# Kernel optimization log

Hardware: AMD Instinct MI355X
Metric: run time of the kernel (lower is better)

Reference implementation:

```python
import jax, jax.numpy as jnp
import numpy as np

N_NODES = 50000
N_EDGES = 800000
D_FEAT = 128
UNITS = 128


def setup_inputs() -> dict:
    key = jax.random.key(0)
    k1, k2, k3, k4 = jax.random.split(key, 4)
    x = jax.random.normal(k1, (N_NODES, D_FEAT), dtype=jnp.float32)
    source = jax.random.randint(k2, (N_EDGES,), 0, N_NODES, dtype=jnp.int32)
    target = jax.random.randint(k3, (N_EDGES,), 0, N_NODES, dtype=jnp.int32)
    W = jax.random.normal(k4, (D_FEAT, UNITS), dtype=jnp.float32) * (1.0 / np.sqrt(D_FEAT))
    b = jnp.zeros((UNITS,), dtype=jnp.float32)
    return {"x": x, "source": source, "target": target, "W": W, "b": b}


def _degree(idx, n_nodes):
    # in/out degree = segment-sum of unit edge weights; clamp to >= 1 (no self loops)
    deg = jnp.zeros((n_nodes,), dtype=jnp.float32).at[idx].add(1.0)
    return jnp.maximum(deg, 1.0)


def reference(x, source, target, W, b):
    n = x.shape[0]
    # degree_normalization == "in_out": sender scale from out-degree, receiver from in-degree
    sender_scale = jax.lax.rsqrt(_degree(source, n))[:, None]      # [N, 1]
    receiver_scale = jax.lax.rsqrt(_degree(target, n))[:, None]    # [N, 1]
    normalized = sender_scale * x                                  # [N, D]
    source_bcast = normalized[source]                              # [E, D] gather
    pooled = jax.ops.segment_sum(source_bcast, target, num_segments=n)  # [N, D] scatter-add
    pooled = receiver_scale * pooled
    # Dense(units, activation='relu', use_bias=True)
    return jax.nn.relu(pooled @ W + b)
```

## Files before the change

kernel.cpp:

```cpp
#include <hip/hip_runtime.h>
#include <hip/hip_bf16.h>

#define N_FEAT 128
#define EPT 8
#define CHUNK 2048
#define BSHIFT 8
#define MAXRANGE 256
#define CAP 8192
#define LSTR 66

typedef short bf16x8 __attribute__((ext_vector_type(8)));
typedef float f32x4  __attribute__((ext_vector_type(4)));

__device__ __forceinline__ unsigned short f2bf_rtne(float f) {
    unsigned u = __float_as_uint(f);
    u += 0x7fffu + ((u >> 16) & 1u);
    return (unsigned short)(u >> 16);
}
__device__ __forceinline__ float bf2f(unsigned short h) {
    return __uint_as_float((unsigned)h << 16);
}

__global__ __launch_bounds__(256) void scatter_kernel(const int* __restrict__ source,
                                                      const int* __restrict__ target,
                                                      int* __restrict__ curT,
                                                      int* __restrict__ curS,
                                                      unsigned int* __restrict__ pairsT,
                                                      unsigned char* __restrict__ srcB,
                                                      int E, int NB) {
    __shared__ unsigned int   lds_pairs[CHUNK];
    __shared__ unsigned short lds_sp[CHUNK];
    __shared__ int ct[MAXRANGE], cs[MAXRANGE];
    __shared__ int st[MAXRANGE], ss[MAXRANGE];
    __shared__ int gt[MAXRANGE], gs[MAXRANGE];
    int tid = threadIdx.x, b = blockIdx.x;
    int base = b * CHUNK;
    int cnt = E - base; if (cnt > CHUNK) cnt = CHUNK;

    int rs[EPT], rt[EPT];
    ct[tid] = 0; cs[tid] = 0;
    __syncthreads();
    #pragma unroll
    for (int j = 0; j < EPT; ++j) {
        int e = base + j * 256 + tid;
        if (e < E) {
            int s = source[e], t = target[e];
            rs[j] = s; rt[j] = t;
            atomicAdd(&ct[t >> BSHIFT], 1);
            atomicAdd(&cs[s >> BSHIFT], 1);
        }
    }
    __syncthreads();
    int vt = ct[tid], vs = cs[tid];
    st[tid] = vt; ss[tid] = vs;
    __syncthreads();
    #pragma unroll
    for (int off = 1; off < 256; off <<= 1) {
        int t1 = (tid >= off) ? st[tid - off] : 0;
        int t2 = (tid >= off) ? ss[tid - off] : 0;
        __syncthreads();
        st[tid] += t1; ss[tid] += t2;
        __syncthreads();
    }
    int et = st[tid] - vt, es = ss[tid] - vs;
    int gT = 0, gS = 0;
    if (tid < NB) {
        if (vt) gT = atomicAdd(&curT[tid], vt);
        if (vs) gS = atomicAdd(&curS[tid], vs);
    }
    __syncthreads();
    st[tid] = et; ss[tid] = es;
    ct[tid] = et; cs[tid] = es;
    gt[tid] = gT; gs[tid] = gS;
    __syncthreads();
    #pragma unroll
    for (int j = 0; j < EPT; ++j) {
        int e = base + j * 256 + tid;
        if (e < E) {
            int s = rs[j], t = rt[j];
            int k = t >> BSHIFT;
            int p = atomicAdd(&ct[k], 1);
            lds_pairs[p] = (unsigned)s | ((unsigned)t << 16);
            int k2 = s >> BSHIFT;
            int p2 = atomicAdd(&cs[k2], 1);
            lds_sp[p2] = (unsigned short)s;
        }
    }
    __syncthreads();
    for (int i = tid; i < cnt; i += 256) {
        unsigned w = lds_pairs[i];
        int k = w >> 24;
        pairsT[(size_t)k * CAP + gt[k] + (i - st[k])] = w;
        unsigned short sp = lds_sp[i];
        int k2 = sp >> 8;
        srcB[(size_t)k2 * CAP + gs[k2] + (i - ss[k2])] = (unsigned char)sp;
    }
}

__global__ __launch_bounds__(256) void prep_kernel(const unsigned char* __restrict__ srcB,
                                                   const unsigned int* __restrict__ pairsT,
                                                   const int* __restrict__ curT,
                                                   const int* __restrict__ curS,
                                                   const float* __restrict__ x,
                                                   const float* __restrict__ W,
                                                   unsigned short* __restrict__ xb,
                                                   int2* __restrict__ offs,
                                                   int* __restrict__ elist,
                                                   float* __restrict__ ri,
                                                   unsigned short* __restrict__ Whi,
                                                   unsigned short* __restrict__ Wlo,
                                                   int N, int NB) {
    __shared__ int hist[MAXRANGE];
    __shared__ int sb[MAXRANGE];
    __shared__ int excl[MAXRANGE];
    __shared__ int cur[MAXRANGE];
    __shared__ float so_l[MAXRANGE];
    int tid = threadIdx.x, b = blockIdx.x;

    if (b < NB) {
        hist[tid] = 0;
        __syncthreads();
        int cnt = curS[b];
        size_t base = (size_t)b * CAP;
        for (int i = tid; i < cnt; i += 256)
            atomicAdd(&hist[srcB[base + i]], 1);
        __syncthreads();
        {
            int d = hist[tid]; if (d < 1) d = 1;
            so_l[tid] = rsqrtf((float)d);
        }
        __syncthreads();
        int row0 = b << BSHIFT;
        int nrows = N - row0; if (nrows > 256) nrows = 256;
        if (nrows <= 0) return;
        int nf4 = nrows * (N_FEAT / 4);
        const float4* xr = (const float4*)(x + (size_t)row0 * N_FEAT);
        ushort4* xo = (ushort4*)(xb + (size_t)row0 * N_FEAT);
        for (int i = tid; i < nf4; i += 256) {
            float s = so_l[i >> 5];
            float4 v = xr[i];
            xo[i] = make_ushort4(f2bf_rtne(s * v.x), f2bf_rtne(s * v.y),
                                 f2bf_rtne(s * v.z), f2bf_rtne(s * v.w));
        }
    } else if (b < 2 * NB) {
        int bb = b - NB;
        hist[tid] = 0; cur[tid] = 0;
        __syncthreads();
        int cnt = curT[bb];
        int gbase = bb * CAP;
        for (int i = tid; i < cnt; i += 256)
            atomicAdd(&hist[(pairsT[(size_t)gbase + i] >> 16) & 255], 1);
        __syncthreads();
        int deg = hist[tid];
        sb[tid] = deg;
        __syncthreads();
        #pragma unroll
        for (int off = 1; off < 256; off <<= 1) {
            int t = (tid >= off) ? sb[tid - off] : 0;
            __syncthreads();
            sb[tid] += t;
            __syncthreads();
        }
        excl[tid] = sb[tid] - deg;
        __syncthreads();
        int node = (bb << BSHIFT) + tid;
        if (node < N) {
            int st0 = gbase + excl[tid];
            offs[node] = make_int2(st0, st0 + deg);
            int d = deg; if (d < 1) d = 1;
            ri[node] = rsqrtf((float)d);
        }
        for (int i = tid; i < cnt; i += 256) {
            unsigned w = pairsT[(size_t)gbase + i];
            int tl = (w >> 16) & 255;
            int pos = atomicAdd(&cur[tl], 1);
            elist[gbase + excl[tl] + pos] = (int)(w & 0xFFFFu);
        }
    } else {
        int idx = (b - 2 * NB) * 256 + tid;
        int lane = idx & 63;
        int ks = (idx >> 6) & 3;
        int ct2 = idx >> 8;
        int n  = ct2 * 16 + (lane & 15);
        int k0 = ks * 32 + (lane >> 4) * 8;
        unsigned short h[8], l[8];
        #pragma unroll
        for (int j = 0; j < 8; ++j) {
            float w = W[(k0 + j) * N_FEAT + n];
            unsigned short hh = f2bf_rtne(w);
            h[j] = hh;
            l[j] = f2bf_rtne(w - bf2f(hh));
        }
        size_t off = (size_t)idx * 8;
        *(ushort4*)(Whi + off)     = make_ushort4(h[0], h[1], h[2], h[3]);
        *(ushort4*)(Whi + off + 4) = make_ushort4(h[4], h[5], h[6], h[7]);
        *(ushort4*)(Wlo + off)     = make_ushort4(l[0], l[1], l[2], l[3]);
        *(ushort4*)(Wlo + off + 4) = make_ushort4(l[4], l[5], l[6], l[7]);
    }
}

#define ACC_ROW(u, a) { a.x += __uint_as_float((u) << 16); \
                        a.y += __uint_as_float((u) & 0xffff0000u); }

__global__ __launch_bounds__(256) void agg_gemm_kernel(const unsigned short* __restrict__ xb,
                                                       const int* __restrict__ elist,
                                                       const int2* __restrict__ offs,
                                                       const float* __restrict__ ri,
                                                       const unsigned short* __restrict__ Whi,
                                                       const unsigned short* __restrict__ Wlo,
                                                       const float* __restrict__ bias,
                                                       float* __restrict__ out,
                                                       int N) {
    __shared__ unsigned int hi_l[16 * LSTR];
    __shared__ unsigned int lo_l[16 * LSTR];
    int wave = threadIdx.x >> 6;
    int lane = threadIdx.x & 63;
    int quad = lane >> 4;
    int rowbase = blockIdx.x * 16;
    int col = lane * 2;

    #pragma unroll
    for (int i = 0; i < 4; ++i) {
        int r = wave * 4 + i;
        int node = rowbase + r;
        float vx = 0.f, vy = 0.f;
        if (node < N) {
            int2 oe = offs[node];
            int start = __builtin_amdgcn_readfirstlane(oe.x);
            int end   = __builtin_amdgcn_readfirstlane(oe.y);
            float rr = ri[node];
            float2 a0 = make_float2(0.f, 0.f), a1 = a0, a2 = a0, a3 = a0;
            int j = start;
            for (; j + 16 <= end; j += 16) {
                int e0 = elist[j],      e1 = elist[j + 1];
                int e2 = elist[j + 2],  e3 = elist[j + 3];
                int e4 = elist[j + 4],  e5 = elist[j + 5];
                int e6 = elist[j + 6],  e7 = elist[j + 7];
                int e8 = elist[j + 8],  e9 = elist[j + 9];
                int ea = elist[j + 10], eb = elist[j + 11];
                int ec = elist[j + 12], ed = elist[j + 13];
                int ee = elist[j + 14], ef = elist[j + 15];
                unsigned u0 = *(const unsigned*)(xb + (size_t)e0 * N_FEAT + col);
                unsigned u1 = *(const unsigned*)(xb + (size_t)e1 * N_FEAT + col);
                unsigned u2 = *(const unsigned*)(xb + (size_t)e2 * N_FEAT + col);
                unsigned u3 = *(const unsigned*)(xb + (size_t)e3 * N_FEAT + col);
                unsigned u4 = *(const unsigned*)(xb + (size_t)e4 * N_FEAT + col);
                unsigned u5 = *(const unsigned*)(xb + (size_t)e5 * N_FEAT + col);
                unsigned u6 = *(const unsigned*)(xb + (size_t)e6 * N_FEAT + col);
                unsigned u7 = *(const unsigned*)(xb + (size_t)e7 * N_FEAT + col);
                unsigned u8 = *(const unsigned*)(xb + (size_t)e8 * N_FEAT + col);
                unsigned u9 = *(const unsigned*)(xb + (size_t)e9 * N_FEAT + col);
                unsigned ua = *(const unsigned*)(xb + (size_t)ea * N_FEAT + col);
                unsigned ub = *(const unsigned*)(xb + (size_t)eb * N_FEAT + col);
                unsigned uc = *(const unsigned*)(xb + (size_t)ec * N_FEAT + col);
                unsigned ud = *(const unsigned*)(xb + (size_t)ed * N_FEAT + col);
                unsigned ue = *(const unsigned*)(xb + (size_t)ee * N_FEAT + col);
                unsigned uf = *(const unsigned*)(xb + (size_t)ef * N_FEAT + col);
                ACC_ROW(u0, a0) ACC_ROW(u1, a1) ACC_ROW(u2, a2) ACC_ROW(u3, a3)
                ACC_ROW(u4, a0) ACC_ROW(u5, a1) ACC_ROW(u6, a2) ACC_ROW(u7, a3)
                ACC_ROW(u8, a0) ACC_ROW(u9, a1) ACC_ROW(ua, a2) ACC_ROW(ub, a3)
                ACC_ROW(uc, a0) ACC_ROW(ud, a1) ACC_ROW(ue, a2) ACC_ROW(uf, a3)
            }
            for (; j + 8 <= end; j += 8) {
                int e0 = elist[j],     e1 = elist[j + 1];
                int e2 = elist[j + 2], e3 = elist[j + 3];
                int e4 = elist[j + 4], e5 = elist[j + 5];
                int e6 = elist[j + 6], e7 = elist[j + 7];
                unsigned u0 = *(const unsigned*)(xb + (size_t)e0 * N_FEAT + col);
                unsigned u1 = *(const unsigned*)(xb + (size_t)e1 * N_FEAT + col);
                unsigned u2 = *(const unsigned*)(xb + (size_t)e2 * N_FEAT + col);
                unsigned u3 = *(const unsigned*)(xb + (size_t)e3 * N_FEAT + col);
                unsigned u4 = *(const unsigned*)(xb + (size_t)e4 * N_FEAT + col);
                unsigned u5 = *(const unsigned*)(xb + (size_t)e5 * N_FEAT + col);
                unsigned u6 = *(const unsigned*)(xb + (size_t)e6 * N_FEAT + col);
                unsigned u7 = *(const unsigned*)(xb + (size_t)e7 * N_FEAT + col);
                ACC_ROW(u0, a0) ACC_ROW(u1, a1) ACC_ROW(u2, a2) ACC_ROW(u3, a3)
                ACC_ROW(u4, a0) ACC_ROW(u5, a1) ACC_ROW(u6, a2) ACC_ROW(u7, a3)
            }
            for (; j < end; ++j) {
                int e = elist[j];
                unsigned u = *(const unsigned*)(xb + (size_t)e * N_FEAT + col);
                ACC_ROW(u, a0)
            }
            vx = ((a0.x + a1.x) + (a2.x + a3.x)) * rr;
            vy = ((a0.y + a1.y) + (a2.y + a3.y)) * rr;
        }
        unsigned short hx = f2bf_rtne(vx), hy = f2bf_rtne(vy);
        unsigned short lx = f2bf_rtne(vx - bf2f(hx)), ly = f2bf_rtne(vy - bf2f(hy));
        hi_l[r * LSTR + lane] = (unsigned)hx | ((unsigned)hy << 16);
        lo_l[r * LSTR + lane] = (unsigned)lx | ((unsigned)ly << 16);
    }
    __syncthreads();

    bf16x8 Ahi[4], Alo[4];
    int m = lane & 15;
    #pragma unroll
    for (int ks = 0; ks < 4; ++ks) {
        int a = m * LSTR + ks * 16 + quad * 4;
        Ahi[ks] = *(const bf16x8*)(hi_l + a);
        Alo[ks] = *(const bf16x8*)(lo_l + a);
    }
    const bf16x8* BH = (const bf16x8*)Whi;
    const bf16x8* BL = (const bf16x8*)Wlo;

    #pragma unroll
    for (int c = 0; c < 2; ++c) {
        int ct = wave * 2 + c;
        f32x4 acc = {0.f, 0.f, 0.f, 0.f};
        #pragma unroll
        for (int ks = 0; ks < 4; ++ks) {
            bf16x8 bh = BH[(ct * 4 + ks) * 64 + lane];
            bf16x8 bl = BL[(ct * 4 + ks) * 64 + lane];
            acc = __builtin_amdgcn_mfma_f32_16x16x32_bf16(Ahi[ks], bh, acc, 0, 0, 0);
            acc = __builtin_amdgcn_mfma_f32_16x16x32_bf16(Alo[ks], bh, acc, 0, 0, 0);
            acc = __builtin_amdgcn_mfma_f32_16x16x32_bf16(Ahi[ks], bl, acc, 0, 0, 0);
        }
        int colc = ct * 16 + m;
        float bv = bias[colc];
        #pragma unroll
        for (int reg = 0; reg < 4; ++reg) {
            int r = rowbase + quad * 4 + reg;
            if (r < N)
                out[(size_t)r * N_FEAT + colc] = fmaxf(acc[reg] + bv, 0.f);
        }
    }
}

extern "C" void kernel_launch(void* const* d_in, const int* in_sizes, int n_in,
                              void* d_out, int out_size, void* d_ws, size_t ws_size,
                              hipStream_t stream) {
    const float* x      = (const float*)d_in[0];
    const int*   source = (const int*)d_in[1];
    const int*   target = (const int*)d_in[2];
    const float* W      = (const float*)d_in[3];
    const float* bias   = (const float*)d_in[4];
    float*       out    = (float*)d_out;

    const int N = in_sizes[0] / N_FEAT;
    const int E = in_sizes[1];

    const int NB   = (N + MAXRANGE - 1) >> BSHIFT;
    const int NBLK = (E + CHUNK - 1) / CHUNK;

    uintptr_t p = (uintptr_t)d_ws;
    auto carve = [&](size_t bytes) {
        p = (p + 255) & ~(uintptr_t)255;
        uintptr_t r = p;
        p += bytes;
        return (void*)r;
    };
    int*            curs    = (int*)carve((size_t)2 * NB * sizeof(int));
    int*            curT    = curs;
    int*            curS    = curs + NB;
    unsigned int*   pairsT  = (unsigned int*)carve((size_t)NB * CAP * sizeof(unsigned int));
    int*            elist   = (int*)carve((size_t)NB * CAP * sizeof(int));
    unsigned char*  srcB    = (unsigned char*)carve((size_t)NB * CAP);
    float*          ri      = (float*)carve((size_t)N * sizeof(float));
    int2*           offs    = (int2*)carve((size_t)N * sizeof(int2));
    unsigned short* xb      = (unsigned short*)carve((size_t)N * N_FEAT * sizeof(unsigned short));
    unsigned short* Whi     = (unsigned short*)carve((size_t)N_FEAT * N_FEAT * sizeof(unsigned short));
    unsigned short* Wlo     = (unsigned short*)carve((size_t)N_FEAT * N_FEAT * sizeof(unsigned short));
    (void)ws_size; (void)n_in; (void)out_size;

    (void)hipMemsetAsync(curs, 0, (size_t)2 * NB * sizeof(int), stream);

    scatter_kernel<<<NBLK, 256, 0, stream>>>(source, target, curT, curS, pairsT, srcB, E, NB);
    prep_kernel<<<2 * NB + 8, 256, 0, stream>>>(srcB, pairsT, curT, curS, x, W,
                                                xb, offs, elist, ri, Whi, Wlo, N, NB);
    agg_gemm_kernel<<<(N + 15) / 16, 256, 0, stream>>>(xb, elist, offs, ri,
                                                       Whi, Wlo, bias, out, N);
}
```

Before: 153.1 us.

## Count out-degree with global atomics and gather 16-byte rows per lane

The scatter kernel no longer bins source indices into byte buckets. It increments a per-node global out-degree array with atomics, which removes the srcB buffer and the histogram pass in prep. The x prescale/bf16 conversion becomes a separate grid-stride branch reading the degree directly. The aggregation loop now has each quarter-wave handle a different edge, loading 16-byte chunks of a row and combining partial sums with cross-lane shuffles. The trade is contended global atomics and extra shuffle work in exchange for wider gathers and fewer passes.

```diff
diff --git a/kernel.cpp b/kernel.cpp
--- a/kernel.cpp
+++ b/kernel.cpp
@@ -8,6 +8,7 @@
 #define MAXRANGE 256
 #define CAP 8192
 #define LSTR 66
+#define PA_BLOCKS 1024
 
 typedef short bf16x8 __attribute__((ext_vector_type(8)));
 typedef float f32x4  __attribute__((ext_vector_type(4)));
@@ -24,21 +25,19 @@
 __global__ __launch_bounds__(256) void scatter_kernel(const int* __restrict__ source,
                                                       const int* __restrict__ target,
                                                       int* __restrict__ curT,
-                                                      int* __restrict__ curS,
+                                                      int* __restrict__ degS,
                                                       unsigned int* __restrict__ pairsT,
-                                                      unsigned char* __restrict__ srcB,
                                                       int E, int NB) {
-    __shared__ unsigned int   lds_pairs[CHUNK];
-    __shared__ unsigned short lds_sp[CHUNK];
-    __shared__ int ct[MAXRANGE], cs[MAXRANGE];
-    __shared__ int st[MAXRANGE], ss[MAXRANGE];
-    __shared__ int gt[MAXRANGE], gs[MAXRANGE];
+    __shared__ unsigned int lds_pairs[CHUNK];
+    __shared__ int ct[MAXRANGE];
+    __shared__ int st[MAXRANGE];
+    __shared__ int gt[MAXRANGE];
     int tid = threadIdx.x, b = blockIdx.x;
     int base = b * CHUNK;
     int cnt = E - base; if (cnt > CHUNK) cnt = CHUNK;
 
     int rs[EPT], rt[EPT];
-    ct[tid] = 0; cs[tid] = 0;
+    ct[tid] = 0;
     __syncthreads();
     #pragma unroll
     for (int j = 0; j < EPT; ++j) {
@@ -47,43 +46,34 @@
             int s = source[e], t = target[e];
             rs[j] = s; rt[j] = t;
             atomicAdd(&ct[t >> BSHIFT], 1);
-            atomicAdd(&cs[s >> BSHIFT], 1);
-        }
-    }
-    __syncthreads();
-    int vt = ct[tid], vs = cs[tid];
-    st[tid] = vt; ss[tid] = vs;
+            atomicAdd(&degS[s], 1);
+        }
+    }
+    __syncthreads();
+    int vt = ct[tid];
+    st[tid] = vt;
     __syncthreads();
     #pragma unroll
     for (int off = 1; off < 256; off <<= 1) {
         int t1 = (tid >= off) ? st[tid - off] : 0;
-        int t2 = (tid >= off) ? ss[tid - off] : 0;
-        __syncthreads();
-        st[tid] += t1; ss[tid] += t2;
-        __syncthreads();
-    }
-    int et = st[tid] - vt, es = ss[tid] - vs;
-    int gT = 0, gS = 0;
-    if (tid < NB) {
-        if (vt) gT = atomicAdd(&curT[tid], vt);
-        if (vs) gS = atomicAdd(&curS[tid], vs);
-    }
-    __syncthreads();
-    st[tid] = et; ss[tid] = es;
-    ct[tid] = et; cs[tid] = es;
-    gt[tid] = gT; gs[tid] = gS;
+        __syncthreads();
+        st[tid] += t1;
+        __syncthreads();
+    }
+    int et = st[tid] - vt;
+    int gT = 0;
+    if (tid < NB && vt) gT = atomicAdd(&curT[tid], vt);
+    __syncthreads();
+    st[tid] = et; ct[tid] = et; gt[tid] = gT;
     __syncthreads();
     #pragma unroll
     for (int j = 0; j < EPT; ++j) {
         int e = base + j * 256 + tid;
         if (e < E) {
-            int s = rs[j], t = rt[j];
+            int t = rt[j];
             int k = t >> BSHIFT;
             int p = atomicAdd(&ct[k], 1);
-            lds_pairs[p] = (unsigned)s | ((unsigned)t << 16);
-            int k2 = s >> BSHIFT;
-            int p2 = atomicAdd(&cs[k2], 1);
-            lds_sp[p2] = (unsigned short)s;
+            lds_pairs[p] = (unsigned)rs[j] | ((unsigned)t << 16);
         }
     }
     __syncthreads();
@@ -91,16 +81,12 @@
         unsigned w = lds_pairs[i];
         int k = w >> 24;
         pairsT[(size_t)k * CAP + gt[k] + (i - st[k])] = w;
-        unsigned short sp = lds_sp[i];
-        int k2 = sp >> 8;
-        srcB[(size_t)k2 * CAP + gs[k2] + (i - ss[k2])] = (unsigned char)sp;
-    }
-}
-
-__global__ __launch_bounds__(256) void prep_kernel(const unsigned char* __restrict__ srcB,
-                                                   const unsigned int* __restrict__ pairsT,
+    }
+}
+
+__global__ __launch_bounds__(256) void prep_kernel(const unsigned int* __restrict__ pairsT,
                                                    const int* __restrict__ curT,
-                                                   const int* __restrict__ curS,
+                                                   const int* __restrict__ degS,
                                                    const float* __restrict__ x,
                                                    const float* __restrict__ W,
                                                    unsigned short* __restrict__ xb,
@@ -114,36 +100,10 @@
     __shared__ int sb[MAXRANGE];
     __shared__ int excl[MAXRANGE];
     __shared__ int cur[MAXRANGE];
-    __shared__ float so_l[MAXRANGE];
     int tid = threadIdx.x, b = blockIdx.x;
 
     if (b < NB) {
-        hist[tid] = 0;
-        __syncthreads();
-        int cnt = curS[b];
-        size_t base = (size_t)b * CAP;
-        for (int i = tid; i < cnt; i += 256)
-            atomicAdd(&hist[srcB[base + i]], 1);
-        __syncthreads();
-        {
-            int d = hist[tid]; if (d < 1) d = 1;
-            so_l[tid] = rsqrtf((float)d);
-        }
-        __syncthreads();
-        int row0 = b << BSHIFT;
-        int nrows = N - row0; if (nrows > 256) nrows = 256;
-        if (nrows <= 0) return;
-        int nf4 = nrows * (N_FEAT / 4);
-        const float4* xr = (const float4*)(x + (size_t)row0 * N_FEAT);
-        ushort4* xo = (ushort4*)(xb + (size_t)row0 * N_FEAT);
-        for (int i = tid; i < nf4; i += 256) {
-            float s = so_l[i >> 5];
-            float4 v = xr[i];
-            xo[i] = make_ushort4(f2bf_rtne(s * v.x), f2bf_rtne(s * v.y),
-                                 f2bf_rtne(s * v.z), f2bf_rtne(s * v.w));
-        }
-    } else if (b < 2 * NB) {
-        int bb = b - NB;
+        int bb = b;
         hist[tid] = 0; cur[tid] = 0;
         __syncthreads();
         int cnt = curT[bb];
@@ -176,8 +136,8 @@
             int pos = atomicAdd(&cur[tl], 1);
             elist[gbase + excl[tl] + pos] = (int)(w & 0xFFFFu);
         }
-    } else {
-        int idx = (b - 2 * NB) * 256 + tid;
+    } else if (b < NB + 8) {
+        int idx = (b - NB) * 256 + tid;
         int lane = idx & 63;
         int ks = (idx >> 6) & 3;
         int ct2 = idx >> 8;
@@ -196,6 +156,19 @@
         *(ushort4*)(Whi + off + 4) = make_ushort4(h[4], h[5], h[6], h[7]);
         *(ushort4*)(Wlo + off)     = make_ushort4(l[0], l[1], l[2], l[3]);
         *(ushort4*)(Wlo + off + 4) = make_ushort4(l[4], l[5], l[6], l[7]);
+    } else {
+        int pb = b - NB - 8;
+        int total = N * (N_FEAT / 4);
+        const float4* xr = (const float4*)x;
+        ushort4* xo = (ushort4*)xb;
+        for (int i = pb * 256 + tid; i < total; i += PA_BLOCKS * 256) {
+            int row = i >> 5;
+            int d = degS[row]; if (d < 1) d = 1;
+            float s = rsqrtf((float)d);
+            float4 v = xr[i];
+            xo[i] = make_ushort4(f2bf_rtne(s * v.x), f2bf_rtne(s * v.y),
+                                 f2bf_rtne(s * v.z), f2bf_rtne(s * v.w));
+        }
     }
 }
 
@@ -216,14 +189,14 @@
     int wave = threadIdx.x >> 6;
     int lane = threadIdx.x & 63;
     int quad = lane >> 4;
+    int k16  = lane & 15;
     int rowbase = blockIdx.x * 16;
-    int col = lane * 2;
+    const uint4* xr = (const uint4*)xb;
 
     #pragma unroll
     for (int i = 0; i < 4; ++i) {
         int r = wave * 4 + i;
         int node = rowbase + r;
-        float vx = 0.f, vy = 0.f;
         if (node < N) {
             int2 oe = offs[node];
             int start = __builtin_amdgcn_readfirstlane(oe.x);
@@ -232,68 +205,67 @@
             float2 a0 = make_float2(0.f, 0.f), a1 = a0, a2 = a0, a3 = a0;
             int j = start;
             for (; j + 16 <= end; j += 16) {
-                int e0 = elist[j],      e1 = elist[j + 1];
-                int e2 = elist[j + 2],  e3 = elist[j + 3];
-                int e4 = elist[j + 4],  e5 = elist[j + 5];
-                int e6 = elist[j + 6],  e7 = elist[j + 7];
-                int e8 = elist[j + 8],  e9 = elist[j + 9];
-                int ea = elist[j + 10], eb = elist[j + 11];
-                int ec = elist[j + 12], ed = elist[j + 13];
-                int ee = elist[j + 14], ef = elist[j + 15];
-                unsigned u0 = *(const unsigned*)(xb + (size_t)e0 * N_FEAT + col);
-                unsigned u1 = *(const unsigned*)(xb + (size_t)e1 * N_FEAT + col);
-                unsigned u2 = *(const unsigned*)(xb + (size_t)e2 * N_FEAT + col);
-                unsigned u3 = *(const unsigned*)(xb + (size_t)e3 * N_FEAT + col);
-                unsigned u4 = *(const unsigned*)(xb + (size_t)e4 * N_FEAT + col);
-                unsigned u5 = *(const unsigned*)(xb + (size_t)e5 * N_FEAT + col);
-                unsigned u6 = *(const unsigned*)(xb + (size_t)e6 * N_FEAT + col);
-                unsigned u7 = *(const unsigned*)(xb + (size_t)e7 * N_FEAT + col);
-                unsigned u8 = *(const unsigned*)(xb + (size_t)e8 * N_FEAT + col);
-                unsigned u9 = *(const unsigned*)(xb + (size_t)e9 * N_FEAT + col);
-                unsigned ua = *(const unsigned*)(xb + (size_t)ea * N_FEAT + col);
-                unsigned ub = *(const unsigned*)(xb + (size_t)eb * N_FEAT + col);
-                unsigned uc = *(const unsigned*)(xb + (size_t)ec * N_FEAT + col);
-                unsigned ud = *(const unsigned*)(xb + (size_t)ed * N_FEAT + col);
-                unsigned ue = *(const unsigned*)(xb + (size_t)ee * N_FEAT + col);
-                unsigned uf = *(const unsigned*)(xb + (size_t)ef * N_FEAT + col);
-                ACC_ROW(u0, a0) ACC_ROW(u1, a1) ACC_ROW(u2, a2) ACC_ROW(u3, a3)
-                ACC_ROW(u4, a0) ACC_ROW(u5, a1) ACC_ROW(u6, a2) ACC_ROW(u7, a3)
-                ACC_ROW(u8, a0) ACC_ROW(u9, a1) ACC_ROW(ua, a2) ACC_ROW(ub, a3)
-                ACC_ROW(uc, a0) ACC_ROW(ud, a1) ACC_ROW(ue, a2) ACC_ROW(uf, a3)
-            }
-            for (; j + 8 <= end; j += 8) {
-                int e0 = elist[j],     e1 = elist[j + 1];
-                int e2 = elist[j + 2], e3 = elist[j + 3];
-                int e4 = elist[j + 4], e5 = elist[j + 5];
-                int e6 = elist[j + 6], e7 = elist[j + 7];
-                unsigned u0 = *(const unsigned*)(xb + (size_t)e0 * N_FEAT + col);
-                unsigned u1 = *(const unsigned*)(xb + (size_t)e1 * N_FEAT + col);
-                unsigned u2 = *(const unsigned*)(xb + (size_t)e2 * N_FEAT + col);
-                unsigned u3 = *(const unsigned*)(xb + (size_t)e3 * N_FEAT + col);
-                unsigned u4 = *(const unsigned*)(xb + (size_t)e4 * N_FEAT + col);
-                unsigned u5 = *(const unsigned*)(xb + (size_t)e5 * N_FEAT + col);
-                unsigned u6 = *(const unsigned*)(xb + (size_t)e6 * N_FEAT + col);
-                unsigned u7 = *(const unsigned*)(xb + (size_t)e7 * N_FEAT + col);
-                ACC_ROW(u0, a0) ACC_ROW(u1, a1) ACC_ROW(u2, a2) ACC_ROW(u3, a3)
-                ACC_ROW(u4, a0) ACC_ROW(u5, a1) ACC_ROW(u6, a2) ACC_ROW(u7, a3)
-            }
-            for (; j < end; ++j) {
-                int e = elist[j];
-                unsigned u = *(const unsigned*)(xb + (size_t)e * N_FEAT + col);
-                ACC_ROW(u, a0)
-            }
-            vx = ((a0.x + a1.x) + (a2.x + a3.x)) * rr;
-            vy = ((a0.y + a1.y) + (a2.y + a3.y)) * rr;
-        }
-        unsigned short hx = f2bf_rtne(vx), hy = f2bf_rtne(vy);
-        unsigned short lx = f2bf_rtne(vx - bf2f(hx)), ly = f2bf_rtne(vy - bf2f(hy));
-        hi_l[r * LSTR + lane] = (unsigned)hx | ((unsigned)hy << 16);
-        lo_l[r * LSTR + lane] = (unsigned)lx | ((unsigned)ly << 16);
+                int e0 = elist[j + quad];
+                int e1 = elist[j + 4 + quad];
+                int e2 = elist[j + 8 + quad];
+                int e3 = elist[j + 12 + quad];
+                uint4 u0 = xr[e0 * 16 + k16];
+                uint4 u1 = xr[e1 * 16 + k16];
+                uint4 u2 = xr[e2 * 16 + k16];
+                uint4 u3 = xr[e3 * 16 + k16];
+                ACC_ROW(u0.x, a0) ACC_ROW(u0.y, a1) ACC_ROW(u0.z, a2) ACC_ROW(u0.w, a3)
+                ACC_ROW(u1.x, a0) ACC_ROW(u1.y, a1) ACC_ROW(u1.z, a2) ACC_ROW(u1.w, a3)
+                ACC_ROW(u2.x, a0) ACC_ROW(u2.y, a1) ACC_ROW(u2.z, a2) ACC_ROW(u2.w, a3)
+                ACC_ROW(u3.x, a0) ACC_ROW(u3.y, a1) ACC_ROW(u3.z, a2) ACC_ROW(u3.w, a3)
+            }
+            for (; j + 4 <= end; j += 4) {
+                int e = elist[j + quad];
+                uint4 u = xr[e * 16 + k16];
+                ACC_ROW(u.x, a0) ACC_ROW(u.y, a1) ACC_ROW(u.z, a2) ACC_ROW(u.w, a3)
+            }
+            if (j < end) {
+                int jj = j + quad;
+                bool valid = jj < end;
+                int e = valid ? elist[jj] : 0;
+                uint4 u = xr[e * 16 + k16];
+                if (valid) {
+                    ACC_ROW(u.x, a0) ACC_ROW(u.y, a1) ACC_ROW(u.z, a2) ACC_ROW(u.w, a3)
+                }
+            }
+            float v[8] = { a0.x, a0.y, a1.x, a1.y, a2.x, a2.y, a3.x, a3.y };
+            #pragma unroll
+            for (int t = 0; t < 8; ++t) {
+                v[t] += __shfl_xor(v[t], 16);
+                v[t] += __shfl_xor(v[t], 32);
+                v[t] *= rr;
+            }
+            if (quad == 0) {
+                unsigned hp[4], lp[4];
+                #pragma unroll
+                for (int t = 0; t < 4; ++t) {
+                    unsigned short h0 = f2bf_rtne(v[2 * t]);
+                    unsigned short h1 = f2bf_rtne(v[2 * t + 1]);
+                    unsigned short l0 = f2bf_rtne(v[2 * t]     - bf2f(h0));
+                    unsigned short l1 = f2bf_rtne(v[2 * t + 1] - bf2f(h1));
+                    hp[t] = (unsigned)h0 | ((unsigned)h1 << 16);
+                    lp[t] = (unsigned)l0 | ((unsigned)l1 << 16);
+                }
+                unsigned int* hd = hi_l + r * LSTR + 4 * k16;
+                unsigned int* ld = lo_l + r * LSTR + 4 * k16;
+                hd[0] = hp[0]; hd[1] = hp[1]; hd[2] = hp[2]; hd[3] = hp[3];
+                ld[0] = lp[0]; ld[1] = lp[1]; ld[2] = lp[2]; ld[3] = lp[3];
+            }
+        } else if (quad == 0) {
+            unsigned int* hd = hi_l + r * LSTR + 4 * k16;
+            unsigned int* ld = lo_l + r * LSTR + 4 * k16;
+            hd[0] = 0; hd[1] = 0; hd[2] = 0; hd[3] = 0;
+            ld[0] = 0; ld[1] = 0; ld[2] = 0; ld[3] = 0;
+        }
     }
     __syncthreads();
 
     bf16x8 Ahi[4], Alo[4];
-    int m = lane & 15;
+    int m = k16;
     #pragma unroll
     for (int ks = 0; ks < 4; ++ks) {
         int a = m * LSTR + ks * 16 + quad * 4;
@@ -319,9 +291,9 @@
         float bv = bias[colc];
         #pragma unroll
         for (int reg = 0; reg < 4; ++reg) {
-            int r = rowbase + quad * 4 + reg;
-            if (r < N)
-                out[(size_t)r * N_FEAT + colc] = fmaxf(acc[reg] + bv, 0.f);
+            int rr2 = rowbase + quad * 4 + reg;
+            if (rr2 < N)
+                out[(size_t)rr2 * N_FEAT + colc] = fmaxf(acc[reg] + bv, 0.f);
         }
     }
 }
@@ -349,12 +321,10 @@
         p += bytes;
         return (void*)r;
     };
-    int*            curs    = (int*)carve((size_t)2 * NB * sizeof(int));
-    int*            curT    = curs;
-    int*            curS    = curs + NB;
+    int*            curT    = (int*)carve((size_t)(NB + N) * sizeof(int));
+    int*            degS    = curT + NB;
     unsigned int*   pairsT  = (unsigned int*)carve((size_t)NB * CAP * sizeof(unsigned int));
-    int*            elist   = (int*)carve((size_t)NB * CAP * sizeof(int));
-    unsigned char*  srcB    = (unsigned char*)carve((size_t)NB * CAP);
+    int*            elist   = (int*)carve((size_t)NB * CAP * sizeof(int) + 64);
     float*          ri      = (float*)carve((size_t)N * sizeof(float));
     int2*           offs    = (int2*)carve((size_t)N * sizeof(int2));
     unsigned short* xb      = (unsigned short*)carve((size_t)N * N_FEAT * sizeof(unsigned short));
@@ -362,11 +332,11 @@
     unsigned short* Wlo     = (unsigned short*)carve((size_t)N_FEAT * N_FEAT * sizeof(unsigned short));
     (void)ws_size; (void)n_in; (void)out_size;
 
-    (void)hipMemsetAsync(curs, 0, (size_t)2 * NB * sizeof(int), stream);
-
-    scatter_kernel<<<NBLK, 256, 0, stream>>>(source, target, curT, curS, pairsT, srcB, E, NB);
-    prep_kernel<<<2 * NB + 8, 256, 0, stream>>>(srcB, pairsT, curT, curS, x, W,
-                                                xb, offs, elist, ri, Whi, Wlo, N, NB);
+    (void)hipMemsetAsync(curT, 0, (size_t)(NB + N) * sizeof(int), stream);
+
+    scatter_kernel<<<NBLK, 256, 0, stream>>>(source, target, curT, degS, pairsT, E, NB);
+    prep_kernel<<<NB + 8 + PA_BLOCKS, 256, 0, stream>>>(pairsT, curT, degS, x, W,
+                                                        xb, offs, elist, ri, Whi, Wlo, N, NB);
     agg_gemm_kernel<<<(N + 15) / 16, 256, 0, stream>>>(xb, elist, offs, ri,
                                                        Whi, Wlo, bias, out, N);
 }
```

Result: slower. 174.5 us (+14.0%).
